# Optimization experiments

Measured on AMD Instinct MI355X. Metric: run time of the kernel, lower is better.

## Reference

```python
import jax, jax.numpy as jnp
import numpy as np

# Irreps: in1 = in2 = out = 8x0e + 8x1o  (mul_ir / e3nn layout: [scalars(8) | vectors(8,3)])
MUL = 8
DIM = 4 * MUL           # 8*1 + 8*3 = 32
NPATH = 4               # (0e,0e->0e), (1o,1o->0e), (0e,1o->1o), (1o,0e->1o)
WNUM = NPATH * MUL**3   # 2048
BATCH = 1 << 20

# Real O3 Clebsch-Gordan values (component normalization, e3nn convention):
#   C(0e,0e->0e) = 1 ;  C(1o,1o->0e)_ij = delta_ij / sqrt(3)
#   C(0e,1o->1o)_jk = delta_jk ;  C(1o,0e->1o)_ik = delta_ik
INV_SQRT3 = 1.0 / np.sqrt(3.0)
# Path normalization: each output irrep receives 2 paths with fan-in mul*mul each
ALPHA = 1.0 / np.sqrt(2.0 * MUL * MUL)


def setup_inputs() -> dict:
    key = jax.random.key(0)
    k1, k2, k3 = jax.random.split(key, 3)
    x1 = jax.random.normal(k1, (BATCH, DIM), dtype=jnp.float32)
    x2 = jax.random.normal(k2, (BATCH, DIM), dtype=jnp.float32)
    weight = jax.random.normal(k3, (1, WNUM), dtype=jnp.float32)
    return {"x1": x1, "x2": x2, "weight": weight}


def reference(x1, x2, weight):
    B = x1.shape[0]
    n = MUL ** 3
    w = weight[0]
    # per-path fully-connected weights, each (mul1, mul2, mul3)
    W0 = w[0 * n:1 * n].reshape(MUL, MUL, MUL)  # 0e x 0e -> 0e
    W1 = w[1 * n:2 * n].reshape(MUL, MUL, MUL)  # 1o x 1o -> 0e
    W2 = w[2 * n:3 * n].reshape(MUL, MUL, MUL)  # 0e x 1o -> 1o
    W3 = w[3 * n:4 * n].reshape(MUL, MUL, MUL)  # 1o x 0e -> 1o

    s1 = x1[:, :MUL]                       # (B, 8) scalars
    v1 = x1[:, MUL:].reshape(B, MUL, 3)    # (B, 8, 3) vectors
    s2 = x2[:, :MUL]
    v2 = x2[:, MUL:].reshape(B, MUL, 3)

    # 0e output: scalar*scalar path + vector-dot path (CG = delta_ij/sqrt(3))
    out0 = (jnp.einsum('bu,bv,uvw->bw', s1, s2, W0)
            + INV_SQRT3 * jnp.einsum('bui,bvi,uvw->bw', v1, v2, W1))
    # 1o output: scalar*vector paths (CG = identity on the vector index)
    out1 = (jnp.einsum('bu,bvk,uvw->bwk', s1, v2, W2)
            + jnp.einsum('buk,bv,uvw->bwk', v1, s2, W3))

    out = jnp.concatenate([out0, out1.reshape(B, 3 * MUL)], axis=-1)
    return ALPHA * out
```

## Files before the change

kernel.cpp:

```cpp
#include <hip/hip_runtime.h>


constexpr int TPB = 256;

__global__ __launch_bounds__(TPB) void tp_kernel(
    const float* __restrict__ x1,
    const float* __restrict__ x2,
    const float* __restrict__ wg,
    float* __restrict__ out,
    int batch)
{
    const float INV3  = 0.57735026918962576f;
    const float ALPHA = 0.088388347648318447f;

    int b = blockIdx.x * TPB + threadIdx.x;
    if (b >= batch) return;

    float X1[32], X2[32];
    {
        const float4* p1 = (const float4*)(x1 + (size_t)b * 32);
        const float4* p2 = (const float4*)(x2 + (size_t)b * 32);
        #pragma unroll
        for (int j = 0; j < 8; ++j) {
            float4 t1 = p1[j];
            X1[4*j+0] = t1.x; X1[4*j+1] = t1.y; X1[4*j+2] = t1.z; X1[4*j+3] = t1.w;
            float4 t2 = p2[j];
            X2[4*j+0] = t2.x; X2[4*j+1] = t2.y; X2[4*j+2] = t2.z; X2[4*j+3] = t2.w;
        }
    }

    float acc0[8], acc0b[8], acc1[8][3];
    #pragma unroll
    for (int t = 0; t < 8; ++t) {
        acc0[t] = 0.f; acc0b[t] = 0.f;
        acc1[t][0] = 0.f; acc1[t][1] = 0.f; acc1[t][2] = 0.f;
    }

    #pragma unroll
    for (int v = 0; v < 8; ++v) {
        #pragma unroll
        for (int u = 0; u < 8; ++u) {
            float p = X1[u] * X2[v];
            float d = X1[8+u*3+0]*X2[8+v*3+0]
                    + X1[8+u*3+1]*X2[8+v*3+1]
                    + X1[8+u*3+2]*X2[8+v*3+2];
            const float* w0 = wg + (u*64 + v*8);
            #pragma unroll
            for (int t = 0; t < 8; ++t) {
                acc0[t]  += p * w0[t];
                acc0b[t] += d * w0[512 + t];
            }
        }
    }

    #pragma unroll
    for (int v = 0; v < 8; ++v) {
        float a[8];
        #pragma unroll
        for (int t = 0; t < 8; ++t) a[t] = 0.f;
        #pragma unroll
        for (int u = 0; u < 8; ++u) {
            const float* w2 = wg + 1024 + (u*64 + v*8);
            float su = X1[u];
            #pragma unroll
            for (int t = 0; t < 8; ++t) a[t] += su * w2[t];
        }
        float c0 = X2[8+v*3+0], c1 = X2[8+v*3+1], c2 = X2[8+v*3+2];
        #pragma unroll
        for (int t = 0; t < 8; ++t) {
            acc1[t][0] += c0 * a[t];
            acc1[t][1] += c1 * a[t];
            acc1[t][2] += c2 * a[t];
        }
    }

    #pragma unroll
    for (int u = 0; u < 8; ++u) {
        float a[8];
        #pragma unroll
        for (int t = 0; t < 8; ++t) a[t] = 0.f;
        #pragma unroll
        for (int v = 0; v < 8; ++v) {
            const float* w3 = wg + 1536 + (u*64 + v*8);
            float sv = X2[v];
            #pragma unroll
            for (int t = 0; t < 8; ++t) a[t] += sv * w3[t];
        }
        float c0 = X1[8+u*3+0], c1 = X1[8+u*3+1], c2 = X1[8+u*3+2];
        #pragma unroll
        for (int t = 0; t < 8; ++t) {
            acc1[t][0] += c0 * a[t];
            acc1[t][1] += c1 * a[t];
            acc1[t][2] += c2 * a[t];
        }
    }

    float O[32];
    #pragma unroll
    for (int t = 0; t < 8; ++t) O[t] = ALPHA * (acc0[t] + INV3 * acc0b[t]);
    #pragma unroll
    for (int t = 0; t < 8; ++t) {
        O[8 + t*3 + 0] = ALPHA * acc1[t][0];
        O[8 + t*3 + 1] = ALPHA * acc1[t][1];
        O[8 + t*3 + 2] = ALPHA * acc1[t][2];
    }
    float4* po = (float4*)(out + (size_t)b * 32);
    #pragma unroll
    for (int j = 0; j < 8; ++j) {
        po[j] = make_float4(O[4*j+0], O[4*j+1], O[4*j+2], O[4*j+3]);
    }
}

extern "C" void kernel_launch(void* const* d_in, const int* in_sizes, int n_in,
                              void* d_out, int out_size, void* d_ws, size_t ws_size,
                              hipStream_t stream) {
    const float* x1 = (const float*)d_in[0];
    const float* x2 = (const float*)d_in[1];
    const float* wg = (const float*)d_in[2];
    float* out = (float*)d_out;

    int batch = in_sizes[0] / 32;
    dim3 grid((batch + TPB - 1) / TPB), block(TPB);
    hipLaunchKernelGGL(tp_kernel, grid, block, 0, stream, x1, x2, wg, out, batch);
}
```

Before: 382.8 us.

## Stage weights in LDS and fuse path-2 loop into path-0/1 loop

Each block copies the 2048-float weight tensor into shared memory with float4 loads, then reads the weights as float4 LDS broadcasts instead of uniform global/scalar loads. The path-2 contraction is merged into the first (v,u) loop so its weights are read in the same pass. This targets the latency of repeated weight fetches from global memory. In exchange each block adds 8KB of LDS, a barrier, and a redundant per-block weight copy, and the early return is moved after the barrier.

```diff
diff --git a/kernel.cpp b/kernel.cpp
--- a/kernel.cpp
+++ b/kernel.cpp
@@ -13,8 +13,9 @@
     const float INV3  = 0.57735026918962576f;
     const float ALPHA = 0.088388347648318447f;
 
+    __shared__ alignas(16) float W[2048];
+
     int b = blockIdx.x * TPB + threadIdx.x;
-    if (b >= batch) return;
 
     float X1[32], X2[32];
     {
@@ -29,6 +30,17 @@
         }
     }
 
+    {
+        const float4* ws = (const float4*)wg;
+        float4* wd = (float4*)W;
+        int t = threadIdx.x;
+        wd[t]       = ws[t];
+        wd[t + 256] = ws[t + 256];
+    }
+    __syncthreads();
+
+    if (b >= batch) return;
+
     float acc0[8], acc0b[8], acc1[8][3];
     #pragma unroll
     for (int t = 0; t < 8; ++t) {
@@ -38,60 +50,57 @@
 
     #pragma unroll
     for (int v = 0; v < 8; ++v) {
+        float s2v = X2[v];
+        float c0 = X2[8+v*3+0], c1 = X2[8+v*3+1], c2 = X2[8+v*3+2];
+        float e[8];
+        #pragma unroll
+        for (int t = 0; t < 8; ++t) e[t] = 0.f;
+
         #pragma unroll
         for (int u = 0; u < 8; ++u) {
-            float p = X1[u] * X2[v];
-            float d = X1[8+u*3+0]*X2[8+v*3+0]
-                    + X1[8+u*3+1]*X2[8+v*3+1]
-                    + X1[8+u*3+2]*X2[8+v*3+2];
-            const float* w0 = wg + (u*64 + v*8);
-            #pragma unroll
-            for (int t = 0; t < 8; ++t) {
-                acc0[t]  += p * w0[t];
-                acc0b[t] += d * w0[512 + t];
-            }
+            float s1u = X1[u];
+            float p = s1u * s2v;
+            float d = X1[8+u*3+0]*c0 + X1[8+u*3+1]*c1 + X1[8+u*3+2]*c2;
+            const float4* w0 = (const float4*)&W[u*64 + v*8];
+            const float4* w1 = (const float4*)&W[512 + u*64 + v*8];
+            const float4* w2 = (const float4*)&W[1024 + u*64 + v*8];
+            float4 a0 = w0[0], b0 = w0[1];
+            float4 a1 = w1[0], b1 = w1[1];
+            float4 a2 = w2[0], b2 = w2[1];
+            acc0[0] += p*a0.x; acc0[1] += p*a0.y; acc0[2] += p*a0.z; acc0[3] += p*a0.w;
+            acc0[4] += p*b0.x; acc0[5] += p*b0.y; acc0[6] += p*b0.z; acc0[7] += p*b0.w;
+            acc0b[0] += d*a1.x; acc0b[1] += d*a1.y; acc0b[2] += d*a1.z; acc0b[3] += d*a1.w;
+            acc0b[4] += d*b1.x; acc0b[5] += d*b1.y; acc0b[6] += d*b1.z; acc0b[7] += d*b1.w;
+            e[0] += s1u*a2.x; e[1] += s1u*a2.y; e[2] += s1u*a2.z; e[3] += s1u*a2.w;
+            e[4] += s1u*b2.x; e[5] += s1u*b2.y; e[6] += s1u*b2.z; e[7] += s1u*b2.w;
         }
-    }
-
-    #pragma unroll
-    for (int v = 0; v < 8; ++v) {
-        float a[8];
-        #pragma unroll
-        for (int t = 0; t < 8; ++t) a[t] = 0.f;
-        #pragma unroll
-        for (int u = 0; u < 8; ++u) {
-            const float* w2 = wg + 1024 + (u*64 + v*8);
-            float su = X1[u];
-            #pragma unroll
-            for (int t = 0; t < 8; ++t) a[t] += su * w2[t];
-        }
-        float c0 = X2[8+v*3+0], c1 = X2[8+v*3+1], c2 = X2[8+v*3+2];
         #pragma unroll
         for (int t = 0; t < 8; ++t) {
-            acc1[t][0] += c0 * a[t];
-            acc1[t][1] += c1 * a[t];
-            acc1[t][2] += c2 * a[t];
+            acc1[t][0] += c0 * e[t];
+            acc1[t][1] += c1 * e[t];
+            acc1[t][2] += c2 * e[t];
         }
     }
 
     #pragma unroll
     for (int u = 0; u < 8; ++u) {
-        float a[8];
+        float f[8];
         #pragma unroll
-        for (int t = 0; t < 8; ++t) a[t] = 0.f;
+        for (int t = 0; t < 8; ++t) f[t] = 0.f;
         #pragma unroll
         for (int v = 0; v < 8; ++v) {
-            const float* w3 = wg + 1536 + (u*64 + v*8);
             float sv = X2[v];
-            #pragma unroll
-            for (int t = 0; t < 8; ++t) a[t] += sv * w3[t];
+            const float4* w3 = (const float4*)&W[1536 + u*64 + v*8];
+            float4 a3 = w3[0], b3 = w3[1];
+            f[0] += sv*a3.x; f[1] += sv*a3.y; f[2] += sv*a3.z; f[3] += sv*a3.w;
+            f[4] += sv*b3.x; f[5] += sv*b3.y; f[6] += sv*b3.z; f[7] += sv*b3.w;
         }
         float c0 = X1[8+u*3+0], c1 = X1[8+u*3+1], c2 = X1[8+u*3+2];
         #pragma unroll
         for (int t = 0; t < 8; ++t) {
-            acc1[t][0] += c0 * a[t];
-            acc1[t][1] += c1 * a[t];
-            acc1[t][2] += c2 * a[t];
+            acc1[t][0] += c0 * f[t];
+            acc1[t][1] += c1 * f[t];
+            acc1[t][2] += c2 * f[t];
         }
     }
 
```

Measured after the change: 444.9 us. 1.16x slower.
